# Kernel tuning notes

Measured on AMD Instinct MI355X. Metric: run time of the kernel, lower is better.

## Reference

```python
import jax, jax.numpy as jnp
import numpy as np

B, D, O = 16384, 1024, 2048
MU, LAM = 0.9, 0.1


def setup_inputs() -> dict:
    key = jax.random.key(0)
    ks = jax.random.split(key, 16)
    stdv = float(1.0 / np.sqrt(D))
    u = lambda k, shape, s: jax.random.uniform(k, shape, jnp.float32, -s, s)
    return {
        "x": jax.random.normal(ks[0], (B, D), jnp.float32),
        "x_ctx": jax.random.normal(ks[1], (B, D), jnp.float32),
        "classifier": u(ks[2], (O, D), stdv),
        "none_tensor": u(ks[3], (1, D), stdv),
        "ctx_q_w": u(ks[4], (O, D), stdv),
        "ctx_q_b": u(ks[5], (O,), stdv),
        "word_g_w": u(ks[6], (1, D), stdv),
        "word_g_b": u(ks[7], (1,), stdv),
        "tcq_w1": u(ks[8], (D, D), stdv),
        "tcq_b1": u(ks[9], (D,), stdv),
        "tcq_w2": u(ks[10], (O, D), stdv),
        "tcq_b2": u(ks[11], (O,), stdv),
        "history_input": 0.1 * jax.random.normal(ks[12], (O - 1, D), jnp.float32),
        "history_count": jax.random.randint(ks[13], (O - 1,), 0, 10),
        "labels": jax.random.randint(ks[14], (B,), 0, O),
    }


def reference(x, x_ctx, classifier, none_tensor, ctx_q_w, ctx_q_b,
              word_g_w, word_g_b, tcq_w1, tcq_b1, tcq_w2, tcq_b2,
              history_input, history_count, labels):
    mu, lam = MU, LAM
    # ---- update_history (torch.no_grad), vectorized over classes via segment_sum ----
    xs = jax.lax.stop_gradient(x)
    sums = jax.ops.segment_sum(xs, labels, num_segments=O)               # [O, D]
    counts = jax.ops.segment_sum(jnp.ones((B,), jnp.float32), labels, num_segments=O)  # [O]
    has = counts[1:] > 0                                                  # classes 1..O-1
    cls_mean = sums[1:] / jnp.maximum(counts[1:], 1.0)[:, None]
    hist = jnp.where(has[:, None], mu * history_input + cls_mean, history_input)
    cnt = history_count + has.astype(history_count.dtype)
    # ---- generate_substitute (mu < 1 branch) ----
    denom = 1.0 - jnp.power(mu, jnp.maximum(cnt, 1).astype(jnp.float32))[:, None]
    v = hist * (1.0 - mu) / denom                                        # [O-1, D]
    r_sub = jnp.concatenate([none_tensor, v], axis=0)                    # [O, D]
    ctx_logits = x_ctx @ ctx_q_w.T + ctx_q_b                              # [B, O]
    att_logits = jax.nn.gelu(x @ tcq_w1.T + tcq_b1, approximate=False) @ tcq_w2.T + tcq_b2  # [B, O]
    # ---- gated combine + bilinear classifier (training=True path: w uses ctx_logits) ----
    g_word = jax.nn.sigmoid(x @ word_g_w.T + word_g_b)                    # [B, 1]
    w = g_word * jax.nn.sigmoid(ctx_logits)                               # [B, O]
    # logits = sum(((1-w)*x[:,None,:] + w*r_sub) * classifier, -1), collapsed algebraically
    logits = (1.0 - w) * (x @ classifier.T) + w * jnp.einsum('od,od->o', r_sub, classifier)[None, :]
    # ---- losses on labels >= 0 (mask-weighted means, jit-safe) ----
    mask = (labels >= 0).astype(jnp.float32)
    n = jnp.maximum(mask.sum(), 1.0)
    lsm = jax.nn.log_softmax(logits, axis=-1)
    nll = -jnp.take_along_axis(lsm, jnp.maximum(labels, 0)[:, None], axis=1)[:, 0]
    ce = (mask * nll).sum() / n
    mse_row = jnp.mean((ctx_logits - att_logits) ** 2, axis=-1)
    mse = (mask * mse_row).sum() / n
    return (ce + lam * mse, logits)
```

## Files before the change

### kernel.cpp

```cpp
#include <hip/hip_runtime.h>
#include <cstdint>
#include <cstddef>

#define DEV __device__ __forceinline__

typedef __attribute__((ext_vector_type(4))) float f32x4;
typedef __attribute__((ext_vector_type(8))) short bf16x8;
typedef unsigned short ushort_t;
typedef __attribute__((ext_vector_type(8))) unsigned short ushort8;

static constexpr int B_ = 16384, D_ = 1024, O_ = 2048;
static constexpr float LAM_ = 0.1f;

static constexpr size_t WS_XBF   = 0;
static constexpr size_t WS_XCBF  = WS_XBF   + (size_t)B_ * D_ * 2;
static constexpr size_t WS_HBF   = WS_XCBF  + (size_t)B_ * D_ * 2;
static constexpr size_t WS_CLSBF = WS_HBF   + (size_t)B_ * D_ * 2;
static constexpr size_t WS_CTWBF = WS_CLSBF + (size_t)O_ * D_ * 2;
static constexpr size_t WS_W2BF  = WS_CTWBF + (size_t)O_ * D_ * 2;
static constexpr size_t WS_W1BF  = WS_W2BF  + (size_t)O_ * D_ * 2;
static constexpr size_t WS_SMALL = WS_W1BF  + (size_t)D_ * D_ * 2;
static constexpr size_t SM_COUNTS = 0;
static constexpr size_t SM_TSUM   = 8192;
static constexpr size_t SM_MSE    = 16384;
static constexpr size_t SM_ZERO_BYTES = 82176;
static constexpr size_t SM_S      = 82176;
static constexpr size_t SM_GWORD  = 90368;
static constexpr size_t SM_CEROW  = 155904;
static constexpr size_t WS_CTXBF  = WS_SMALL + 2 * 1024 * 1024;
static constexpr size_t WS_NEED_BIG = WS_CTXBF + (size_t)B_ * O_ * 2;

DEV float wave_sum(float v) {
  #pragma unroll
  for (int o = 32; o; o >>= 1) v += __shfl_xor(v, o, 64);
  return v;
}

DEV ushort_t f2bf1(float f) {
  union { float f; unsigned u; } c{f};
  unsigned r = c.u + 0x7fffu + ((c.u >> 16) & 1u);
  return (ushort_t)(r >> 16);
}

DEV float bf2f(ushort_t u) {
  union { unsigned u; float f; } c{(unsigned)u << 16};
  return c.f;
}

DEV float sigmoidf(float z) { return 1.0f / (1.0f + expf(-z)); }

DEV void gload_lds16(const ushort_t* g, ushort_t* l) {
  __builtin_amdgcn_global_load_lds((const __attribute__((address_space(1))) void*)g,
                                   (__attribute__((address_space(3))) void*)l, 16, 0, 0);
}

DEV void stage2(const ushort_t* __restrict__ s0, ushort_t* slot, int tid) {
  gload_lds16(s0, slot + tid * 8);
  gload_lds16(s0 + 128 * 1024, slot + (tid + 512) * 8);
}

DEV void stage128s(const ushort_t* __restrict__ src, ushort_t* lds_, int tid) {
  int c0 = tid, c1 = tid + 256;
  int q0 = (c0 & 3) ^ ((c0 >> 3) & 3);
  int q1 = (c1 & 3) ^ ((c1 >> 3) & 3);
  gload_lds16(src + (size_t)(c0 >> 2) * 1024 + q0 * 8, lds_ + c0 * 8);
  gload_lds16(src + (size_t)(c1 >> 2) * 1024 + q1 * 8, lds_ + c1 * 8);
}

DEV f32x4 mfma16(bf16x8 a, bf16x8 b, f32x4 c) {
  return __builtin_amdgcn_mfma_f32_16x16x32_bf16(a, b, c, 0, 0, 0);
}

template<int N> DEV void wait_vm() {
  if constexpr (N == 8)      asm volatile("s_waitcnt vmcnt(8)" ::: "memory");
  else if constexpr (N == 4) asm volatile("s_waitcnt vmcnt(4)" ::: "memory");
  else if constexpr (N == 0) asm volatile("s_waitcnt vmcnt(0)" ::: "memory");
}

__global__ __launch_bounds__(256) void f2bf_multi_kernel(
    const float* __restrict__ s0, ushort_t* __restrict__ d0, int c0,
    const float* __restrict__ s1, ushort_t* __restrict__ d1, int c1,
    const float* __restrict__ s2, ushort_t* __restrict__ d2, int c2,
    const float* __restrict__ s3, ushort_t* __restrict__ d3, int c3,
    const float* __restrict__ s4, ushort_t* __restrict__ d4, int c4) {
  int i = blockIdx.x * 256 + threadIdx.x;
  const float* src; ushort_t* dst; int off;
  if (i < c0)      { src = s0; dst = d0; off = i; }
  else if (i < c1) { src = s1; dst = d1; off = i - c0; }
  else if (i < c2) { src = s2; dst = d2; off = i - c1; }
  else if (i < c3) { src = s3; dst = d3; off = i - c2; }
  else if (i < c4) { src = s4; dst = d4; off = i - c3; }
  else return;
  const float4* p = (const float4*)(src + (size_t)off * 8);
  float4 a = p[0], b = p[1];
  ushort8 o;
  o[0] = f2bf1(a.x); o[1] = f2bf1(a.y); o[2] = f2bf1(a.z); o[3] = f2bf1(a.w);
  o[4] = f2bf1(b.x); o[5] = f2bf1(b.y); o[6] = f2bf1(b.z); o[7] = f2bf1(b.w);
  *(ushort8*)(dst + (size_t)off * 8) = o;
}

__global__ __launch_bounds__(256) void rowdot_cvt_kernel(const float* __restrict__ x,
    const float* __restrict__ cls, const float* __restrict__ wg,
    const float* __restrict__ wgb, const int* __restrict__ labels,
    ushort_t* __restrict__ xbf,
    float* __restrict__ tsum, float* __restrict__ counts, float* __restrict__ g_word) {
  int wave = threadIdx.x >> 6, lane = threadIdx.x & 63;
  int row = blockIdx.x * 4 + wave;
  const float* xr = x + (size_t)row * D_;
  int lab = labels[row];
  const float* cr = cls + (size_t)max(lab, 0) * D_;
  float t = 0.f, g = 0.f;
  #pragma unroll
  for (int j = 0; j < 4; ++j) {
    int d = j * 256 + lane * 4;
    float4 xv = *(const float4*)(xr + d);
    float4 cv = *(const float4*)(cr + d);
    float4 wv = *(const float4*)(wg + d);
    t += xv.x * cv.x + xv.y * cv.y + xv.z * cv.z + xv.w * cv.w;
    g += xv.x * wv.x + xv.y * wv.y + xv.z * wv.z + xv.w * wv.w;
    uint2 pk;
    pk.x = (unsigned)f2bf1(xv.x) | ((unsigned)f2bf1(xv.y) << 16);
    pk.y = (unsigned)f2bf1(xv.z) | ((unsigned)f2bf1(xv.w) << 16);
    *(uint2*)(xbf + (size_t)row * D_ + d) = pk;
  }
  t = wave_sum(t); g = wave_sum(g);
  if (lane == 0) {
    if (lab >= 0) {
      atomicAdd(&tsum[lab], t);
      atomicAdd(&counts[lab], 1.0f);
    }
    g_word[row] = sigmoidf(g + wgb[0]);
  }
}

__global__ __launch_bounds__(256) void scls_kernel(const float* __restrict__ cls,
    const float* __restrict__ none_t, const float* __restrict__ hist,
    const int* __restrict__ hcnt, const float* __restrict__ counts,
    const float* __restrict__ tsum, float* __restrict__ s) {
  int wave = threadIdx.x >> 6, lane = threadIdx.x & 63;
  int o = blockIdx.x * 4 + wave;
  if (o >= O_) return;
  const float* cr = cls + (size_t)o * D_;
  const float* src = (o == 0) ? none_t : hist + (size_t)(o - 1) * D_;
  float dv = 0.f;
  #pragma unroll
  for (int j = 0; j < 4; ++j) {
    int d = j * 256 + lane * 4;
    float4 a = *(const float4*)(src + d);
    float4 c = *(const float4*)(cr + d);
    dv += a.x * c.x + a.y * c.y + a.z * c.z + a.w * c.w;
  }
  dv = wave_sum(dv);
  if (lane == 0) {
    if (o == 0) { s[0] = dv; }
    else {
      float co = counts[o];
      bool has = co > 0.f;
      int cnt = hcnt[o - 1] + (has ? 1 : 0);
      float denom = 1.f - powf(0.9f, (float)max(cnt, 1));
      float val = has ? (0.9f * dv + tsum[o] / fmaxf(co, 1.f)) : dv;
      s[o] = (0.1f / denom) * val;
    }
  }
}

template<bool S01, bool S23, int W1, int W3>
DEV void tile8(int t, const ushort_t* __restrict__ sA0, const ushort_t* __restrict__ sB0,
               ushort_t* lds, int tid, int aoff, int boff, f32x4 (&acc)[8][4]) {
  const int k0 = 2 * t, k1 = 2 * t + 1;
  const ushort_t* As0 = lds + (k0 & 3) * 8192;
  const ushort_t* Bs0 = lds + 32768 + (k0 & 3) * 8192;
  const ushort_t* As1 = lds + (k1 & 3) * 8192;
  const ushort_t* Bs1 = lds + 32768 + (k1 & 3) * 8192;
  bf16x8 afr[4], bfr[4];
  #pragma unroll
  for (int n = 0; n < 4; n++) bfr[n] = *(const bf16x8*)&Bs0[boff + n * 512];
  #pragma unroll
  for (int m = 0; m < 4; m++) afr[m] = *(const bf16x8*)&As0[aoff + m * 512];
  if constexpr (S01) stage2(sA0 + (size_t)(2 * t + 3) * 32, lds + ((2 * t + 3) & 3) * 8192, tid);
  __builtin_amdgcn_s_barrier();
  __builtin_amdgcn_s_setprio(1);
  #pragma unroll
  for (int m = 0; m < 4; m++)
    #pragma unroll
    for (int n = 0; n < 4; n++) acc[m][n] = mfma16(afr[m], bfr[n], acc[m][n]);
  __builtin_amdgcn_s_setprio(0);
  __builtin_amdgcn_s_barrier();
  #pragma unroll
  for (int m = 0; m < 4; m++) afr[m] = *(const bf16x8*)&As0[aoff + (m + 4) * 512];
  if constexpr (S01) stage2(sB0 + (size_t)(2 * t + 3) * 32, lds + 32768 + ((2 * t + 3) & 3) * 8192, tid);
  __builtin_amdgcn_s_barrier();
  __builtin_amdgcn_s_setprio(1);
  #pragma unroll
  for (int m = 0; m < 4; m++)
    #pragma unroll
    for (int n = 0; n < 4; n++) acc[m + 4][n] = mfma16(afr[m], bfr[n], acc[m + 4][n]);
  __builtin_amdgcn_s_setprio(0);
  wait_vm<W1>();
  __builtin_amdgcn_s_barrier();
  #pragma unroll
  for (int n = 0; n < 4; n++) bfr[n] = *(const bf16x8*)&Bs1[boff + n * 512];
  #pragma unroll
  for (int m = 0; m < 4; m++) afr[m] = *(const bf16x8*)&As1[aoff + m * 512];
  if constexpr (S23) stage2(sA0 + (size_t)(2 * t + 4) * 32, lds + ((2 * t + 4) & 3) * 8192, tid);
  __builtin_amdgcn_s_barrier();
  __builtin_amdgcn_s_setprio(1);
  #pragma unroll
  for (int m = 0; m < 4; m++)
    #pragma unroll
    for (int n = 0; n < 4; n++) acc[m][n] = mfma16(afr[m], bfr[n], acc[m][n]);
  __builtin_amdgcn_s_setprio(0);
  __builtin_amdgcn_s_barrier();
  #pragma unroll
  for (int m = 0; m < 4; m++) afr[m] = *(const bf16x8*)&As1[aoff + (m + 4) * 512];
  if constexpr (S23) stage2(sB0 + (size_t)(2 * t + 4) * 32, lds + 32768 + ((2 * t + 4) & 3) * 8192, tid);
  __builtin_amdgcn_s_barrier();
  __builtin_amdgcn_s_setprio(1);
  #pragma unroll
  for (int m = 0; m < 4; m++)
    #pragma unroll
    for (int n = 0; n < 4; n++) acc[m + 4][n] = mfma16(afr[m], bfr[n], acc[m + 4][n]);
  __builtin_amdgcn_s_setprio(0);
  wait_vm<W3>();
  __builtin_amdgcn_s_barrier();
}

template<int EPI, int NTSHIFT, bool CTXB>
__global__ __launch_bounds__(512, 2) void gemm8_kernel(
    const ushort_t* __restrict__ A, const ushort_t* __restrict__ Bmat,
    const float* __restrict__ bias, float* __restrict__ fout,
    ushort_t* __restrict__ hout, ushort_t* __restrict__ ctxbf,
    const float* __restrict__ g_word, const float* __restrict__ svec) {
  __shared__ __align__(16) ushort_t lds[65536];
  const int tid = threadIdx.x, lane = tid & 63, wave = tid >> 6;
  const int wr = wave >> 2, wc = wave & 3;
  const int nwg = 64 << NTSHIFT, cpx = nwg >> 3;
  int bid = blockIdx.x;
  int wg = (bid & 7) * cpx + (bid >> 3);
  const int bm = wg >> NTSHIFT, bn = wg & ((1 << NTSHIFT) - 1);
  const int NCOL = 256 << NTSHIFT;
  const int qsrc = (tid & 3) ^ ((tid >> 3) & 3);
  const ushort_t* sA0 = A + ((size_t)bm * 256 + (tid >> 2)) * 1024 + qsrc * 8;
  const ushort_t* sB0 = Bmat + ((size_t)bn * 256 + (tid >> 2)) * 1024 + qsrc * 8;
  const int qrd = (lane >> 4) ^ (((lane & 15) >> 1) & 3);
  const int aoff = (wr * 128 + (lane & 15)) * 32 + qrd * 8;
  const int boff = (wc * 64 + (lane & 15)) * 32 + qrd * 8;
  f32x4 acc[8][4] = {};
  stage2(sA0, lds, tid);
  stage2(sB0, lds + 32768, tid);
  stage2(sA0 + 32, lds + 8192, tid);
  stage2(sB0 + 32, lds + 32768 + 8192, tid);
  stage2(sA0 + 64, lds + 2 * 8192, tid);
  stage2(sB0 + 64, lds + 32768 + 2 * 8192, tid);
  wait_vm<8>();
  __builtin_amdgcn_s_barrier();
  for (int t = 0; t < 14; ++t)
    tile8<true, true, 8, 8>(t, sA0, sB0, lds, tid, aoff, boff, acc);
  tile8<true, false, 8, 4>(14, sA0, sB0, lds, tid, aoff, boff, acc);
  tile8<false, false, 0, -1>(15, sA0, sB0, lds, tid, aoff, boff, acc);
  #pragma unroll
  for (int m = 0; m < 8; m++) {
    #pragma unroll
    for (int i = 0; i < 4; i++) {
      int row = bm * 256 + wr * 128 + m * 16 + (lane >> 4) * 4 + i;
      float gw = 0.f;
      if constexpr (EPI == 3) gw = g_word[row];
      #pragma unroll
      for (int n = 0; n < 4; n++) {
        int col = bn * 256 + wc * 64 + n * 16 + (lane & 15);
        float v = acc[m][n][i];
        if constexpr (EPI == 0) {
          float z = v + bias[col];
          float gl = 0.5f * z * (1.f + erff(z * 0.70710678118f));
          hout[(size_t)row * 1024 + col] = f2bf1(gl);
        } else if constexpr (EPI == 1) {
          float z = v + bias[col];
          if constexpr (CTXB) ctxbf[(size_t)row * O_ + col] = f2bf1(z);
          else                fout[(size_t)row * NCOL + col] = z;
        } else {
          size_t off = (size_t)row * NCOL + col;
          float ctx = CTXB ? bf2f(ctxbf[(size_t)row * O_ + col]) : fout[off];
          float w = gw * sigmoidf(ctx);
          fout[off] = (1.f - w) * v + w * svec[col];
        }
      }
    }
  }
}

template<bool CTXB>
__global__ __launch_bounds__(256, 3) void gemm128_att(
    const ushort_t* __restrict__ A, const ushort_t* __restrict__ Bmat,
    const float* __restrict__ bias, const float* __restrict__ fout,
    const ushort_t* __restrict__ ctxbf, float* __restrict__ mse_row) {
  __shared__ __align__(16) ushort_t As[128 * 32], Bs[128 * 32];
  const int tid = threadIdx.x, lane = tid & 63, wave = tid >> 6;
  const int wr = wave >> 1, wc = wave & 1;
  int bid = blockIdx.x;
  int group = bid >> 7, within = bid & 127;
  int bm = group * 8 + (within & 7);
  int bn = within >> 3;
  f32x4 acc[4][4] = {};
  const ushort_t* Ap = A + (size_t)bm * 128 * 1024;
  const ushort_t* Bp = Bmat + (size_t)bn * 128 * 1024;
  const int r = lane & 15;
  const int qrd8 = ((lane >> 4) ^ ((r >> 1) & 3)) * 8;
  for (int k0 = 0; k0 < 1024; k0 += 32) {
    stage128s(Ap + k0, As, tid);
    stage128s(Bp + k0, Bs, tid);
    asm volatile("s_waitcnt vmcnt(0)" ::: "memory");
    __builtin_amdgcn_s_barrier();
    bf16x8 af[4], bf[4];
    #pragma unroll
    for (int m = 0; m < 4; m++) af[m] = *(const bf16x8*)&As[(wr * 64 + m * 16 + r) * 32 + qrd8];
    #pragma unroll
    for (int n = 0; n < 4; n++) bf[n] = *(const bf16x8*)&Bs[(wc * 64 + n * 16 + r) * 32 + qrd8];
    #pragma unroll
    for (int m = 0; m < 4; m++)
      #pragma unroll
      for (int n = 0; n < 4; n++) acc[m][n] = mfma16(af[m], bf[n], acc[m][n]);
    __builtin_amdgcn_s_barrier();
  }
  #pragma unroll
  for (int m = 0; m < 4; m++) {
    #pragma unroll
    for (int i = 0; i < 4; i++) {
      int row = bm * 128 + wr * 64 + m * 16 + (lane >> 4) * 4 + i;
      float msum = 0.f;
      #pragma unroll
      for (int n = 0; n < 4; n++) {
        int col = bn * 128 + wc * 64 + n * 16 + (lane & 15);
        float att = acc[m][n][i] + bias[col];
        float ctx = CTXB ? bf2f(ctxbf[(size_t)row * O_ + col])
                         : fout[(size_t)row * O_ + col];
        float d = ctx - att;
        msum += d * d;
      }
      #pragma unroll
      for (int o = 1; o < 16; o <<= 1) msum += __shfl_xor(msum, o, 64);
      if ((lane & 15) == 0) atomicAdd(&mse_row[row], msum);
    }
  }
}

__global__ __launch_bounds__(256) void ce_kernel(const float* __restrict__ logits,
    const int* __restrict__ labels, float* __restrict__ ce_row) {
  int row = blockIdx.x, t = threadIdx.x, lane = t & 63, wave = t >> 6;
  const float* lr = logits + (size_t)row * O_;
  float v[8];
  float m = -INFINITY;
  #pragma unroll
  for (int j = 0; j < 8; j++) { v[j] = lr[t + j * 256]; m = fmaxf(m, v[j]); }
  #pragma unroll
  for (int o = 32; o; o >>= 1) m = fmaxf(m, __shfl_xor(m, o, 64));
  __shared__ float red[8];
  if (lane == 0) red[wave] = m;
  __syncthreads();
  m = fmaxf(fmaxf(red[0], red[1]), fmaxf(red[2], red[3]));
  float se = 0.f;
  #pragma unroll
  for (int j = 0; j < 8; j++) se += expf(v[j] - m);
  se = wave_sum(se);
  if (lane == 0) red[4 + wave] = se;
  __syncthreads();
  if (t == 0) {
    float bs = red[4] + red[5] + red[6] + red[7];
    int lab = labels[row];
    float nll = 0.f;
    if (lab >= 0) nll = -(lr[lab] - m - logf(bs));
    ce_row[row] = nll;
  }
}

__global__ __launch_bounds__(256) void finalize_kernel(const float* __restrict__ ce_row,
    const float* __restrict__ mse_row, const int* __restrict__ labels,
    float* __restrict__ out0) {
  int t = threadIdx.x, lane = t & 63, wave = t >> 6;
  float sn = 0.f, sm = 0.f, sc = 0.f;
  for (int i = t; i < B_; i += 256) {
    if (labels[i] >= 0) { sn += ce_row[i]; sm += mse_row[i]; sc += 1.f; }
  }
  sn = wave_sum(sn); sm = wave_sum(sm); sc = wave_sum(sc);
  __shared__ float r0[4], r1[4], r2[4];
  if (lane == 0) { r0[wave] = sn; r1[wave] = sm; r2[wave] = sc; }
  __syncthreads();
  if (t == 0) {
    float a = r0[0] + r0[1] + r0[2] + r0[3];
    float b = r1[0] + r1[1] + r1[2] + r1[3];
    float c = r2[0] + r2[1] + r2[2] + r2[3];
    out0[0] = (a + LAM_ * (b / (float)O_)) / fmaxf(c, 1.f);
  }
}

extern "C" void kernel_launch(void* const* d_in, const int* in_sizes, int n_in,
                              void* d_out, int out_size, void* d_ws, size_t ws_size,
                              hipStream_t stream) {
  const float* x        = (const float*)d_in[0];
  const float* x_ctx    = (const float*)d_in[1];
  const float* cls      = (const float*)d_in[2];
  const float* none_t   = (const float*)d_in[3];
  const float* ctx_q_w  = (const float*)d_in[4];
  const float* ctx_q_b  = (const float*)d_in[5];
  const float* word_g_w = (const float*)d_in[6];
  const float* word_g_b = (const float*)d_in[7];
  const float* w1       = (const float*)d_in[8];
  const float* b1       = (const float*)d_in[9];
  const float* w2       = (const float*)d_in[10];
  const float* b2       = (const float*)d_in[11];
  const float* hist     = (const float*)d_in[12];
  const int*   hcnt     = (const int*)d_in[13];
  const int*   labels   = (const int*)d_in[14];

  float* out  = (float*)d_out;
  float* out1 = out + 1;
  char* ws = (char*)d_ws;

  ushort_t* xbf   = (ushort_t*)(ws + WS_XBF);
  ushort_t* xcbf  = (ushort_t*)(ws + WS_XCBF);
  ushort_t* hbf   = (ushort_t*)(ws + WS_HBF);
  ushort_t* clsbf = (ushort_t*)(ws + WS_CLSBF);
  ushort_t* ctwbf = (ushort_t*)(ws + WS_CTWBF);
  ushort_t* w2bf  = (ushort_t*)(ws + WS_W2BF);
  ushort_t* w1bf  = (ushort_t*)(ws + WS_W1BF);
  float* counts   = (float*)(ws + WS_SMALL + SM_COUNTS);
  float* tsum     = (float*)(ws + WS_SMALL + SM_TSUM);
  float* mse_row  = (float*)(ws + WS_SMALL + SM_MSE);
  float* s        = (float*)(ws + WS_SMALL + SM_S);
  float* g_word   = (float*)(ws + WS_SMALL + SM_GWORD);
  float* ce_row   = (float*)(ws + WS_SMALL + SM_CEROW);
  ushort_t* ctxbf = (ushort_t*)(ws + WS_CTXBF);
  const bool big  = ws_size >= WS_NEED_BIG;

  hipMemsetAsync(ws + WS_SMALL, 0, SM_ZERO_BYTES, stream);

  rowdot_cvt_kernel<<<B_ / 4, 256, 0, stream>>>(x, cls, word_g_w, word_g_b, labels,
                                                xbf, tsum, counts, g_word);
  {
    int n_xc  = B_ * D_ / 8;
    int n_od  = O_ * D_ / 8;
    int n_dd  = D_ * D_ / 8;
    int c0 = n_xc, c1 = c0 + n_od, c2 = c1 + n_od, c3 = c2 + n_od, c4 = c3 + n_dd;
    f2bf_multi_kernel<<<(c4 + 255) / 256, 256, 0, stream>>>(
        x_ctx, xcbf, c0, cls, clsbf, c1, ctx_q_w, ctwbf, c2,
        w2, w2bf, c3, w1, w1bf, c4);
  }

  scls_kernel<<<O_ / 4, 256, 0, stream>>>(cls, none_t, hist, hcnt, counts, tsum, s);

  gemm8_kernel<0, 2, false><<<256, 512, 0, stream>>>(xbf, w1bf, b1, nullptr, hbf,
                                                     nullptr, nullptr, nullptr);
  if (big)
    gemm8_kernel<1, 3, true><<<512, 512, 0, stream>>>(xcbf, ctwbf, ctx_q_b, out1,
                                                      nullptr, ctxbf, nullptr, nullptr);
  else
    gemm8_kernel<1, 3, false><<<512, 512, 0, stream>>>(xcbf, ctwbf, ctx_q_b, out1,
                                                       nullptr, nullptr, nullptr, nullptr);
  if (big)
    gemm128_att<true><<<2048, 256, 0, stream>>>(hbf, w2bf, b2, out1, ctxbf, mse_row);
  else
    gemm128_att<false><<<2048, 256, 0, stream>>>(hbf, w2bf, b2, out1, nullptr, mse_row);
  if (big)
    gemm8_kernel<3, 3, true><<<512, 512, 0, stream>>>(xbf, clsbf, nullptr, out1,
                                                      nullptr, ctxbf, g_word, s);
  else
    gemm8_kernel<3, 3, false><<<512, 512, 0, stream>>>(xbf, clsbf, nullptr, out1,
                                                       nullptr, nullptr, g_word, s);

  ce_kernel<<<B_, 256, 0, stream>>>(out1, labels, ce_row);
  finalize_kernel<<<1, 256, 0, stream>>>(ce_row, mse_row, labels, out);
}
```

Baseline: 428.8 us.

## Fuse x@W1 and x@classifier GEMMs into one kernel over concatenated weights

```diff
diff --git a/kernel.cpp b/kernel.cpp
--- a/kernel.cpp
+++ b/kernel.cpp
@@ -15,11 +15,10 @@
 static constexpr size_t WS_XBF   = 0;
 static constexpr size_t WS_XCBF  = WS_XBF   + (size_t)B_ * D_ * 2;
 static constexpr size_t WS_HBF   = WS_XCBF  + (size_t)B_ * D_ * 2;
-static constexpr size_t WS_CLSBF = WS_HBF   + (size_t)B_ * D_ * 2;
-static constexpr size_t WS_CTWBF = WS_CLSBF + (size_t)O_ * D_ * 2;
+static constexpr size_t WS_CTWBF = WS_HBF   + (size_t)B_ * D_ * 2;
 static constexpr size_t WS_W2BF  = WS_CTWBF + (size_t)O_ * D_ * 2;
-static constexpr size_t WS_W1BF  = WS_W2BF  + (size_t)O_ * D_ * 2;
-static constexpr size_t WS_SMALL = WS_W1BF  + (size_t)D_ * D_ * 2;
+static constexpr size_t WS_BCOMB = WS_W2BF  + (size_t)O_ * D_ * 2;
+static constexpr size_t WS_SMALL = WS_BCOMB + (size_t)(D_ + O_) * D_ * 2;
 static constexpr size_t SM_COUNTS = 0;
 static constexpr size_t SM_TSUM   = 8192;
 static constexpr size_t SM_MSE    = 16384;
@@ -288,6 +287,73 @@
   }
 }
 
+__global__ __launch_bounds__(512, 2) void hxc_kernel(
+    const ushort_t* __restrict__ A, const ushort_t* __restrict__ Bmat,
+    const float* __restrict__ b1, float* __restrict__ fout,
+    ushort_t* __restrict__ hout, const ushort_t* __restrict__ ctxbf,
+    const float* __restrict__ g_word, const float* __restrict__ svec) {
+  __shared__ __align__(16) ushort_t lds[65536];
+  const int tid = threadIdx.x, lane = tid & 63, wave = tid >> 6;
+  const int wr = wave >> 2, wc = wave & 3;
+  const int nwg = 768, cpx = nwg >> 3;
+  int bid = blockIdx.x;
+  int wg = (bid & 7) * cpx + (bid >> 3);
+  const int bm = wg / 12, bn = wg % 12;
+  const int qsrc = (tid & 3) ^ ((tid >> 3) & 3);
+  const ushort_t* sA0 = A + ((size_t)bm * 256 + (tid >> 2)) * 1024 + qsrc * 8;
+  const ushort_t* sB0 = Bmat + ((size_t)bn * 256 + (tid >> 2)) * 1024 + qsrc * 8;
+  const int qrd = (lane >> 4) ^ (((lane & 15) >> 1) & 3);
+  const int aoff = (wr * 128 + (lane & 15)) * 32 + qrd * 8;
+  const int boff = (wc * 64 + (lane & 15)) * 32 + qrd * 8;
+  f32x4 acc[8][4] = {};
+  stage2(sA0, lds, tid);
+  stage2(sB0, lds + 32768, tid);
+  stage2(sA0 + 32, lds + 8192, tid);
+  stage2(sB0 + 32, lds + 32768 + 8192, tid);
+  stage2(sA0 + 64, lds + 2 * 8192, tid);
+  stage2(sB0 + 64, lds + 32768 + 2 * 8192, tid);
+  wait_vm<8>();
+  __builtin_amdgcn_s_barrier();
+  for (int t = 0; t < 14; ++t)
+    tile8<true, true, 8, 8>(t, sA0, sB0, lds, tid, aoff, boff, acc);
+  tile8<true, false, 8, 4>(14, sA0, sB0, lds, tid, aoff, boff, acc);
+  tile8<false, false, 0, -1>(15, sA0, sB0, lds, tid, aoff, boff, acc);
+  if (bn < 4) {
+    #pragma unroll
+    for (int m = 0; m < 8; m++) {
+      #pragma unroll
+      for (int i = 0; i < 4; i++) {
+        int row = bm * 256 + wr * 128 + m * 16 + (lane >> 4) * 4 + i;
+        #pragma unroll
+        for (int n = 0; n < 4; n++) {
+          int col = bn * 256 + wc * 64 + n * 16 + (lane & 15);
+          float z = acc[m][n][i] + b1[col];
+          float gl = 0.5f * z * (1.f + erff(z * 0.70710678118f));
+          hout[(size_t)row * 1024 + col] = f2bf1(gl);
+        }
+      }
+    }
+  } else {
+    const int bnx = bn - 4;
+    #pragma unroll
+    for (int m = 0; m < 8; m++) {
+      #pragma unroll
+      for (int i = 0; i < 4; i++) {
+        int row = bm * 256 + wr * 128 + m * 16 + (lane >> 4) * 4 + i;
+        float gw = g_word[row];
+        #pragma unroll
+        for (int n = 0; n < 4; n++) {
+          int col = bnx * 256 + wc * 64 + n * 16 + (lane & 15);
+          size_t off = (size_t)row * O_ + col;
+          float ctx = bf2f(ctxbf[off]);
+          float w = gw * sigmoidf(ctx);
+          fout[off] = (1.f - w) * acc[m][n][i] + w * svec[col];
+        }
+      }
+    }
+  }
+}
+
 template<bool CTXB>
 __global__ __launch_bounds__(256, 3) void gemm128_att(
     const ushort_t* __restrict__ A, const ushort_t* __restrict__ Bmat,
@@ -418,10 +484,10 @@
   ushort_t* xbf   = (ushort_t*)(ws + WS_XBF);
   ushort_t* xcbf  = (ushort_t*)(ws + WS_XCBF);
   ushort_t* hbf   = (ushort_t*)(ws + WS_HBF);
-  ushort_t* clsbf = (ushort_t*)(ws + WS_CLSBF);
   ushort_t* ctwbf = (ushort_t*)(ws + WS_CTWBF);
   ushort_t* w2bf  = (ushort_t*)(ws + WS_W2BF);
-  ushort_t* w1bf  = (ushort_t*)(ws + WS_W1BF);
+  ushort_t* bcomb = (ushort_t*)(ws + WS_BCOMB);
+  ushort_t* clspart = bcomb + (size_t)D_ * D_;
   float* counts   = (float*)(ws + WS_SMALL + SM_COUNTS);
   float* tsum     = (float*)(ws + WS_SMALL + SM_TSUM);
   float* mse_row  = (float*)(ws + WS_SMALL + SM_MSE);
@@ -436,35 +502,29 @@
   rowdot_cvt_kernel<<<B_ / 4, 256, 0, stream>>>(x, cls, word_g_w, word_g_b, labels,
                                                 xbf, tsum, counts, g_word);
   {
-    int n_xc  = B_ * D_ / 8;
-    int n_od  = O_ * D_ / 8;
-    int n_dd  = D_ * D_ / 8;
-    int c0 = n_xc, c1 = c0 + n_od, c2 = c1 + n_od, c3 = c2 + n_od, c4 = c3 + n_dd;
+    int n_xc = B_ * D_ / 8, n_od = O_ * D_ / 8, n_dd = D_ * D_ / 8;
+    int c0 = n_xc, c1 = c0 + n_od, c2 = c1 + n_od, c3 = c2 + n_dd, c4 = c3 + n_od;
     f2bf_multi_kernel<<<(c4 + 255) / 256, 256, 0, stream>>>(
-        x_ctx, xcbf, c0, cls, clsbf, c1, ctx_q_w, ctwbf, c2,
-        w2, w2bf, c3, w1, w1bf, c4);
+        x_ctx, xcbf, c0, ctx_q_w, ctwbf, c1, w2, w2bf, c2,
+        w1, bcomb, c3, cls, clspart, c4);
   }
 
   scls_kernel<<<O_ / 4, 256, 0, stream>>>(cls, none_t, hist, hcnt, counts, tsum, s);
 
-  gemm8_kernel<0, 2, false><<<256, 512, 0, stream>>>(xbf, w1bf, b1, nullptr, hbf,
-                                                     nullptr, nullptr, nullptr);
-  if (big)
+  if (big) {
     gemm8_kernel<1, 3, true><<<512, 512, 0, stream>>>(xcbf, ctwbf, ctx_q_b, out1,
                                                       nullptr, ctxbf, nullptr, nullptr);
-  else
+    hxc_kernel<<<768, 512, 0, stream>>>(xbf, bcomb, b1, out1, hbf, ctxbf, g_word, s);
+    gemm128_att<true><<<2048, 256, 0, stream>>>(hbf, w2bf, b2, out1, ctxbf, mse_row);
+  } else {
     gemm8_kernel<1, 3, false><<<512, 512, 0, stream>>>(xcbf, ctwbf, ctx_q_b, out1,
                                                        nullptr, nullptr, nullptr, nullptr);
-  if (big)
-    gemm128_att<true><<<2048, 256, 0, stream>>>(hbf, w2bf, b2, out1, ctxbf, mse_row);
-  else
+    gemm8_kernel<0, 2, false><<<256, 512, 0, stream>>>(xbf, bcomb, b1, nullptr, hbf,
+                                                       nullptr, nullptr, nullptr);
     gemm128_att<false><<<2048, 256, 0, stream>>>(hbf, w2bf, b2, out1, nullptr, mse_row);
-  if (big)
-    gemm8_kernel<3, 3, true><<<512, 512, 0, stream>>>(xbf, clsbf, nullptr, out1,
-                                                      nullptr, ctxbf, g_word, s);
-  else
-    gemm8_kernel<3, 3, false><<<512, 512, 0, stream>>>(xbf, clsbf, nullptr, out1,
+    gemm8_kernel<3, 3, false><<<512, 512, 0, stream>>>(xbf, clspart, nullptr, out1,
                                                        nullptr, nullptr, g_word, s);
+  }
 
   ce_kernel<<<B_, 256, 0, stream>>>(out1, labels, ce_row);
   finalize_kernel<<<1, 256, 0, stream>>>(ce_row, mse_row, labels, out);
```

Measured after the change: 428.3 us. No clear change (-0.1%).
